# Kernel tuning notes

Measured on AMD Instinct MI355X. Metric: run time of the kernel, lower is better.

## Reference

```python
import jax, jax.numpy as jnp
import numpy as np

N_SRC_F = 40000; N_TGT_F = 40000; N_F = N_SRC_F + N_TGT_F
N_SRC_C = 1024; N_TGT_C = 1024; N_C = N_SRC_C + N_TGT_C
NN = 30        # KPConv neighbors per point
K = 15         # kernel points
C1 = 128       # fine-level feats (first_feats_dim)
C2 = 256       # coarse encoder out dim
GNN = 256      # gnn_feats_dim
HEADS = 4
DGCNN_K = 10
FINAL = 32     # final_feats_dim
EXT_F = 1.0; EXT_C = 2.0   # KPConv influence extents (scaled to unit-cube clouds)
EPS = 1e-12


def kpconv(q_pts, s_pts, s_feats, neighb, kpts, W, extent):
    # q_pts [Nq,3], s_pts [Ns,3], s_feats [Ns,Cin], neighb [Nq,NN], kpts [K,3], W [K,Cin,Cout]
    npts = s_pts[neighb]                              # [Nq,NN,3] irregular gather
    rel = npts - q_pts[:, None, :]
    # ||rel - kp||^2 expanded to avoid a [Nq,NN,K,3] intermediate
    d2 = (jnp.sum(rel * rel, -1)[:, :, None] + jnp.sum(kpts * kpts, -1)[None, None, :]
          - 2.0 * jnp.einsum('njd,kd->njk', rel, kpts))
    infl = jax.nn.relu(1.0 - jnp.sqrt(jnp.maximum(d2, EPS)) / extent)   # [Nq,NN,K]
    nf = s_feats[neighb]                              # [Nq,NN,Cin]
    h = jnp.einsum('njk,njc->nkc', infl, nf)          # kernel-point aggregation
    return jnp.einsum('nkc,kcd->nd', h, W)


def knn_idx(coords, k):
    sq = jnp.sum(coords * coords, -1)
    d2 = sq[:, None] + sq[None, :] - 2.0 * (coords @ coords.T)
    return jax.lax.top_k(-d2, k)[1]


def self_layer(coords, x, W, b):
    # DGCNN edge conv: knn on coords, edge = [x_i, x_j - x_i], 1x1 conv + relu, max over k
    idx = knn_idx(coords, DGCNN_K)
    neigh = x[idx]                                    # [N,k,C]
    ctr = jnp.broadcast_to(x[:, None, :], neigh.shape)
    edge = jnp.concatenate([ctr, neigh - ctr], -1)    # [N,k,2C]
    return jnp.max(jax.nn.relu(edge @ W + b), axis=1)


def cross_layer(x, y, Wq, Wk, Wv, Wm, bm):
    # multi-head cross attention x <- y, residual MLP on [x, message]
    N, C = x.shape
    dh = C // HEADS
    q = (x @ Wq).reshape(N, HEADS, dh)
    k = (y @ Wk).reshape(-1, HEADS, dh)
    v = (y @ Wv).reshape(-1, HEADS, dh)
    attn = jax.nn.softmax(jnp.einsum('nhd,mhd->hnm', q, k) / float(np.sqrt(dh)), axis=-1)
    msg = jnp.einsum('hnm,mhd->nhd', attn, v).reshape(N, C)
    return x + jnp.concatenate([x, msg], -1) @ Wm + bm


def l2norm(x):
    return x / jnp.maximum(jnp.linalg.norm(x, axis=1, keepdims=True), EPS)


def _forward(points_f, points_c, features, kernel_points_f, kernel_points_c,
             W_kp1, W_kp2, W_bottle, b_bottle, W_self1, b_self1,
             Wq, Wk, Wv, W_cross, b_cross, W_self2, b_self2,
             W_proj, b_proj, W_score, b_score, epsilon, W_dec, b_dec,
             neighbors_f, pool_idx, upsample_idx, len_src_c):
    # --- encoder: fine KPConv + strided KPConv to coarse ---
    x_f = kpconv(points_f, points_f, features, neighbors_f, kernel_points_f, W_kp1, EXT_F)  # [N_f,C1]
    skip = x_f
    x_c = kpconv(points_c, points_f, x_f, pool_idx, kernel_points_c, W_kp2, EXT_C)          # [N_c,C2]
    feats_c = x_c @ W_bottle + b_bottle                # bottleneck 1x1 conv -> [N_c,GNN]
    src, tgt = feats_c[:len_src_c], feats_c[len_src_c:]
    sc, tc = points_c[:len_src_c], points_c[len_src_c:]
    # --- GCN: self -> cross -> self (weights shared across src/tgt) ---
    src = self_layer(sc, src, W_self1, b_self1)
    tgt = self_layer(tc, tgt, W_self1, b_self1)
    src2 = cross_layer(src, tgt, Wq, Wk, Wv, W_cross, b_cross)
    tgt2 = cross_layer(tgt, src, Wq, Wk, Wv, W_cross, b_cross)
    src = self_layer(sc, src2, W_self2, b_self2)
    tgt = self_layer(tc, tgt2, W_self2, b_self2)
    feats = jnp.concatenate([src, tgt], 0) @ W_proj + b_proj   # proj_gnn
    scores_c_raw = feats @ W_score + b_score                   # proj_score [N_c,1]
    feats_norm = l2norm(feats)
    # --- bidirectional temperature-softmax matching head ---
    ip = feats_norm[:len_src_c] @ feats_norm[len_src_c:].T     # [Ns,Nt]
    temperature = jnp.exp(epsilon) + 0.03
    s1 = jax.nn.softmax(ip / temperature, axis=1) @ scores_c_raw[len_src_c:]
    s2 = jax.nn.softmax(ip.T / temperature, axis=1) @ scores_c_raw[:len_src_c]
    scores_saliency = jnp.concatenate([s1, s2], 0)
    # condition=True, add_cross_overlap=True branch
    x = jnp.concatenate([scores_c_raw, scores_saliency, feats], 1)    # [N_c, GNN+2]
    # --- decoder: nearest upsample + skip concat + unary conv ---
    x = jnp.concatenate([x[upsample_idx], skip], 1)            # [N_f, GNN+2+C1]
    x = x @ W_dec + b_dec                                      # [N_f, FINAL+2]
    feats_f = l2norm(x[:, :FINAL])
    so = jnp.clip(jax.nn.sigmoid(x[:, FINAL]), 0.0, 1.0)
    ss = jnp.clip(jax.nn.sigmoid(x[:, FINAL + 1]), 0.0, 1.0)
    so = jnp.where(jnp.isnan(so) | jnp.isinf(so), 0.0, so)     # regular_score
    ss = jnp.where(jnp.isnan(ss) | jnp.isinf(ss), 0.0, ss)
    return feats_f, so, ss


def _p(k, shape, fan):
    return jax.random.normal(k, shape, jnp.float32) / float(np.sqrt(fan))


def setup_inputs() -> dict:
    key = jax.random.key(0)
    ks = jax.random.split(key, 24)
    inp = {}
    inp['points_f'] = jax.random.uniform(ks[0], (N_F, 3), jnp.float32)
    inp['points_c'] = jax.random.uniform(ks[1], (N_C, 3), jnp.float32)
    inp['features'] = jnp.ones((N_F, 1), jnp.float32)
    inp['kernel_points_f'] = jax.random.normal(ks[2], (K, 3), jnp.float32) * 0.3
    inp['kernel_points_c'] = jax.random.normal(ks[3], (K, 3), jnp.float32) * 0.6
    inp['W_kp1'] = _p(ks[4], (K, 1, C1), K)
    inp['W_kp2'] = _p(ks[5], (K, C1, C2), K * C1)
    inp['W_bottle'] = _p(ks[6], (C2, GNN), C2); inp['b_bottle'] = jnp.zeros((GNN,), jnp.float32)
    inp['W_self1'] = _p(ks[7], (2 * GNN, GNN), 2 * GNN); inp['b_self1'] = jnp.zeros((GNN,), jnp.float32)
    inp['Wq'] = _p(ks[8], (GNN, GNN), GNN)
    inp['Wk'] = _p(ks[9], (GNN, GNN), GNN)
    inp['Wv'] = _p(ks[10], (GNN, GNN), GNN)
    inp['W_cross'] = _p(ks[11], (2 * GNN, GNN), 2 * GNN); inp['b_cross'] = jnp.zeros((GNN,), jnp.float32)
    inp['W_self2'] = _p(ks[12], (2 * GNN, GNN), 2 * GNN); inp['b_self2'] = jnp.zeros((GNN,), jnp.float32)
    inp['W_proj'] = _p(ks[13], (GNN, GNN), GNN); inp['b_proj'] = jnp.zeros((GNN,), jnp.float32)
    inp['W_score'] = _p(ks[14], (GNN, 1), GNN); inp['b_score'] = jnp.zeros((1,), jnp.float32)
    inp['epsilon'] = jnp.array(-5.0, jnp.float32)
    inp['W_dec'] = _p(ks[15], (GNN + 2 + C1, FINAL + 2), GNN + 2 + C1); inp['b_dec'] = jnp.zeros((FINAL + 2,), jnp.float32)
    inp['neighbors_f'] = jax.random.randint(ks[16], (N_F, NN), 0, N_F)
    inp['pool_idx'] = jax.random.randint(ks[17], (N_C, NN), 0, N_F)
    inp['upsample_idx'] = jax.random.randint(ks[18], (N_F,), 0, N_C)
    inp['len_src_c'] = N_SRC_C
    inp['len_src_f'] = N_SRC_F
    return inp


def reference(points_f, points_c, features, kernel_points_f, kernel_points_c,
              W_kp1, W_kp2, W_bottle, b_bottle, W_self1, b_self1,
              Wq, Wk, Wv, W_cross, b_cross, W_self2, b_self2,
              W_proj, b_proj, W_score, b_score, epsilon, W_dec, b_dec,
              neighbors_f, pool_idx, upsample_idx, len_src_c, len_src_f):
    return _forward(points_f, points_c, features, kernel_points_f, kernel_points_c,
                    W_kp1, W_kp2, W_bottle, b_bottle, W_self1, b_self1,
                    Wq, Wk, Wv, W_cross, b_cross, W_self2, b_self2,
                    W_proj, b_proj, W_score, b_score, epsilon, W_dec, b_dec,
                    neighbors_f, pool_idx, upsample_idx, len_src_c)
```

## Files before the change

kernel.cpp:

```cpp
#include <hip/hip_runtime.h>
#include <math.h>

#define NFINE   80000
#define NCRS    2048
#define NSRC    1024
#define NNB     30
#define KP      15
#define C1D     128
#define C2D     256
#define GD      256
#define DGK     10
#define FINALD  32
#define DECOUT  34

#define NCHUNK  8
#define CHUNK   128
#define TK      16
#define KC      4
#define KSTEP   480
#define GTR     16

__global__ __launch_bounds__(256) void kpconv_fine(
    const float* __restrict__ pts, const float* __restrict__ feat,
    const int* __restrict__ nbr, const float* __restrict__ kp,
    const float* __restrict__ W, float* __restrict__ out)
{
    int t = threadIdx.x, w = t >> 6, lane = t & 63;
    int n = blockIdx.x * 4 + w;
    __shared__ float contrib[4][NNB][17];
    __shared__ float h[4][KP + 1];
    float kx[KP], ky[KP], kz[KP], kk[KP];
#pragma unroll
    for (int k = 0; k < KP; k++) {
        kx[k] = kp[k*3]; ky[k] = kp[k*3+1]; kz[k] = kp[k*3+2];
        kk[k] = kx[k]*kx[k] + ky[k]*ky[k] + kz[k]*kz[k];
    }
    if (lane < NNB) {
        float qx = pts[n*3], qy = pts[n*3+1], qz = pts[n*3+2];
        int id = nbr[n*NNB + lane];
        float rx = pts[id*3]-qx, ry = pts[id*3+1]-qy, rz = pts[id*3+2]-qz;
        float rr = rx*rx + ry*ry + rz*rz;
        float f = feat[id];
#pragma unroll
        for (int k = 0; k < KP; k++) {
            float d2 = rr + kk[k] - 2.f*(rx*kx[k] + ry*ky[k] + rz*kz[k]);
            float infl = fmaxf(1.f - sqrtf(fmaxf(d2, 1e-12f)), 0.f);
            contrib[w][lane][k] = infl * f;
        }
    }
    __syncthreads();
    if (lane < KP) {
        float s = 0.f;
#pragma unroll
        for (int j = 0; j < NNB; j++) s += contrib[w][j][lane];
        h[w][lane] = s;
    }
    __syncthreads();
    float a0 = 0.f, a1 = 0.f;
#pragma unroll
    for (int k = 0; k < KP; k++) {
        float hk = h[w][k];
        a0 += hk * W[k*C1D + lane];
        a1 += hk * W[k*C1D + 64 + lane];
    }
    out[(size_t)n*C1D + lane]      = a0;
    out[(size_t)n*C1D + 64 + lane] = a1;
}

__global__ __launch_bounds__(256) void hh_kernel(
    const float* __restrict__ pc, const float* __restrict__ pf,
    const float* __restrict__ xf, const int* __restrict__ pool,
    const float* __restrict__ kp, float* __restrict__ hhg)
{
    int n = blockIdx.x, t = threadIdx.x;
    __shared__ float kx[KP], ky[KP], kz[KP], kk[KP];
    __shared__ float rel[NNB][4];
    __shared__ int   ids[NNB];
    __shared__ float infl[NNB][KP + 1];
    __shared__ float nf[NNB][C1D];
    if (t < KP) {
        float a = kp[t*3], b = kp[t*3+1], c = kp[t*3+2];
        kx[t] = a; ky[t] = b; kz[t] = c; kk[t] = a*a + b*b + c*c;
    }
    if (t < NNB) {
        int id = pool[n*NNB + t]; ids[t] = id;
        float qx = pc[n*3], qy = pc[n*3+1], qz = pc[n*3+2];
        float rx = pf[id*3]-qx, ry = pf[id*3+1]-qy, rz = pf[id*3+2]-qz;
        rel[t][0] = rx; rel[t][1] = ry; rel[t][2] = rz;
        rel[t][3] = rx*rx + ry*ry + rz*rz;
    }
    __syncthreads();
    for (int i = t; i < NNB*KP; i += 256) {
        int j = i / KP, kq = i % KP;
        float d2 = rel[j][3] + kk[kq]
                 - 2.f*(rel[j][0]*kx[kq] + rel[j][1]*ky[kq] + rel[j][2]*kz[kq]);
        infl[j][kq] = fmaxf(1.f - sqrtf(fmaxf(d2, 1e-12f)) * 0.5f, 0.f);
    }
    for (int i = t; i < NNB*C1D; i += 256) {
        int j = i >> 7, c = i & 127;
        nf[j][c] = xf[(size_t)ids[j]*C1D + c];
    }
    __syncthreads();
    for (int i = t; i < KP*C1D; i += 256) {
        int kq = i >> 7, c = i & 127;
        float s = 0.f;
#pragma unroll
        for (int j = 0; j < NNB; j++) s += infl[j][kq] * nf[j][c];
        hhg[(size_t)n*(KP*C1D) + i] = s;
    }
}

__global__ __launch_bounds__(256) void hh_gemm(
    const float* __restrict__ hhg, const float* __restrict__ W,
    float* __restrict__ pbuf)
{
    int t = threadIdx.x;
    int rg = blockIdx.x >> 2, kc = blockIdx.x & 3;
    int n0 = rg * GTR, kb0 = kc * KSTEP;
    __shared__ float xi[GTR][KSTEP];
    float* xf = &xi[0][0];
    for (int i = t; i < GTR*KSTEP; i += 256) {
        int r = i / KSTEP, c = i - r*KSTEP;
        xf[i] = hhg[(size_t)(n0 + r)*(KP*C1D) + kb0 + c];
    }
    __syncthreads();
    float a[GTR];
#pragma unroll
    for (int r = 0; r < GTR; r++) a[r] = 0.f;
    for (int c = 0; c < KSTEP; c += 4) {
        float w0 = W[(size_t)(kb0+c+0)*C2D + t];
        float w1 = W[(size_t)(kb0+c+1)*C2D + t];
        float w2 = W[(size_t)(kb0+c+2)*C2D + t];
        float w3 = W[(size_t)(kb0+c+3)*C2D + t];
#pragma unroll
        for (int r = 0; r < GTR; r++) {
            float4 xv = *(const float4*)&xi[r][c];
            a[r] += xv.x*w0 + xv.y*w1 + xv.z*w2 + xv.w*w3;
        }
    }
#pragma unroll
    for (int r = 0; r < GTR; r++)
        pbuf[(size_t)kc*NCRS*C2D + (size_t)(n0+r)*C2D + t] = a[r];
}

__global__ __launch_bounds__(256) void bottle_fused(
    const float* __restrict__ pbuf, const float* __restrict__ Wb,
    const float* __restrict__ b, float* __restrict__ out)
{
    int t = threadIdx.x, n0 = blockIdx.x * 4;
    const size_t MN = (size_t)NCRS*C2D;
    __shared__ float xi[4][C2D];
    for (int i = t; i < 4*C2D; i += 256) {
        int r = i >> 8, c = i & 255;
        size_t off = (size_t)(n0+r)*C2D + c;
        xi[r][c] = pbuf[off] + pbuf[MN+off] + pbuf[2*MN+off] + pbuf[3*MN+off];
    }
    __syncthreads();
    float a[4];
#pragma unroll
    for (int r = 0; r < 4; r++) a[r] = 0.f;
    for (int c = 0; c < C2D; c += 4) {
        float w0 = Wb[(c+0)*GD + t];
        float w1 = Wb[(c+1)*GD + t];
        float w2 = Wb[(c+2)*GD + t];
        float w3 = Wb[(c+3)*GD + t];
#pragma unroll
        for (int r = 0; r < 4; r++) {
            float4 xv = *(const float4*)&xi[r][c];
            a[r] += xv.x*w0 + xv.y*w1 + xv.z*w2 + xv.w*w3;
        }
    }
    float bv = b[t];
#pragma unroll
    for (int r = 0; r < 4; r++) out[(size_t)(n0+r)*GD + t] = a[r] + bv;
}

__global__ __launch_bounds__(512) void self_gemm(
    const float* __restrict__ x, const float* __restrict__ W,
    float* __restrict__ Y)
{
    int t = threadIdx.x, n0 = blockIdx.x * 4;
    __shared__ float xi[4][GD];
    for (int i = t; i < 4*GD; i += 512) {
        int r = i >> 8, c = i & 255;
        xi[r][c] = x[(size_t)(n0+r)*GD + c];
    }
    __syncthreads();
    const float* wcol = (t < GD) ? (W + t) : (W + (size_t)GD*GD + (t - GD));
    float a[4];
#pragma unroll
    for (int r = 0; r < 4; r++) a[r] = 0.f;
    for (int c = 0; c < GD; c += 4) {
        float w0 = wcol[(size_t)(c+0)*GD];
        float w1 = wcol[(size_t)(c+1)*GD];
        float w2 = wcol[(size_t)(c+2)*GD];
        float w3 = wcol[(size_t)(c+3)*GD];
#pragma unroll
        for (int r = 0; r < 4; r++) {
            float4 xv = *(const float4*)&xi[r][c];
            a[r] += xv.x*w0 + xv.y*w1 + xv.z*w2 + xv.w*w3;
        }
    }
#pragma unroll
    for (int r = 0; r < 4; r++) Y[(size_t)(n0+r)*512 + t] = a[r];
}

__global__ __launch_bounds__(256) void edge_max(
    const float* __restrict__ Y, const int* __restrict__ knn,
    const float* __restrict__ b, float* __restrict__ out)
{
    int n = blockIdx.x, t = threadIdx.x;
    int base = (n < NSRC) ? 0 : NSRC;
    __shared__ int ids[DGK];
    if (t < DGK) ids[t] = base + knn[n*DGK + t];
    __syncthreads();
    float a  = Y[(size_t)n*512 + t];
    float bn = Y[(size_t)n*512 + GD + t];
    float cst = a - bn + b[t];
    float acc = 0.f;
#pragma unroll
    for (int j = 0; j < DGK; j++) {
        float bj = Y[(size_t)ids[j]*512 + GD + t];
        acc = fmaxf(acc, fmaxf(cst + bj, 0.f));
    }
    out[(size_t)n*GD + t] = acc;
}

__global__ __launch_bounds__(256) void qkv_kernel(
    const float* __restrict__ x, const float* __restrict__ Wq,
    const float* __restrict__ Wk, const float* __restrict__ Wv,
    float* __restrict__ qb, float* __restrict__ kb, float* __restrict__ vb)
{
    int t = threadIdx.x, n0 = blockIdx.x * 4;
    __shared__ float xi[4][GD];
    for (int i = t; i < 4*GD; i += 256) {
        int r = i >> 8, c = i & 255;
        xi[r][c] = x[(size_t)(n0+r)*GD + c];
    }
    __syncthreads();
    const float* Ws[3] = {Wq, Wk, Wv};
    float* outs[3] = {qb, kb, vb};
#pragma unroll
    for (int m = 0; m < 3; m++) {
        const float* W = Ws[m];
        float a[4];
#pragma unroll
        for (int r = 0; r < 4; r++) a[r] = 0.f;
        for (int c = 0; c < GD; c += 4) {
            float w0 = W[(c+0)*GD + t];
            float w1 = W[(c+1)*GD + t];
            float w2 = W[(c+2)*GD + t];
            float w3 = W[(c+3)*GD + t];
#pragma unroll
            for (int r = 0; r < 4; r++) {
                float4 xv = *(const float4*)&xi[r][c];
                a[r] += xv.x*w0 + xv.y*w1 + xv.z*w2 + xv.w*w3;
            }
        }
        float* o = outs[m];
#pragma unroll
        for (int r = 0; r < 4; r++) o[(size_t)(n0+r)*GD + t] = a[r];
    }
}

__global__ __launch_bounds__(256) void knn_kernel(
    const float* __restrict__ pts, int* __restrict__ knn)
{
    int g = blockIdx.x;
    int t = threadIdx.x;
    int base = (g < NSRC) ? 0 : NSRC;
    int local = g - base;
    const float* P = pts + (size_t)base*3;
    __shared__ float d2s[NSRC];
    __shared__ float wval[4];
    __shared__ int   widx[4];
    float qx = P[local*3], qy = P[local*3+1], qz = P[local*3+2];
    float sqn = qx*qx + qy*qy + qz*qz;
#pragma unroll
    for (int ii = 0; ii < 4; ii++) {
        int m = t + ii*256;
        float px = P[m*3], py = P[m*3+1], pz = P[m*3+2];
        float sqm = px*px + py*py + pz*pz;
        d2s[m] = sqn + sqm - 2.f*(qx*px + qy*py + qz*pz);
    }
    __syncthreads();
    for (int r = 0; r < DGK; r++) {
        float bv = 3.4e38f; int bidx = NSRC;
#pragma unroll
        for (int ii = 0; ii < 4; ii++) {
            int m = t + ii*256;
            float v = d2s[m];
            if (v < bv) { bv = v; bidx = m; }
        }
#pragma unroll
        for (int off = 32; off >= 1; off >>= 1) {
            float ov = __shfl_xor(bv, off);
            int   oi = __shfl_xor(bidx, off);
            if (ov < bv || (ov == bv && oi < bidx)) { bv = ov; bidx = oi; }
        }
        if ((t & 63) == 0) { wval[t >> 6] = bv; widx[t >> 6] = bidx; }
        __syncthreads();
        if (t == 0) {
            float fv = wval[0]; int fi = widx[0];
#pragma unroll
            for (int wv2 = 1; wv2 < 4; wv2++)
                if (wval[wv2] < fv || (wval[wv2] == fv && widx[wv2] < fi)) {
                    fv = wval[wv2]; fi = widx[wv2];
                }
            knn[g*DGK + r] = fi;
            d2s[fi] = 3.4e38f;
        }
        __syncthreads();
    }
}

__global__ __launch_bounds__(256) void attn_flash(
    const float* __restrict__ qb, const float* __restrict__ kb,
    const float* __restrict__ vb, float* __restrict__ pm,
    float* __restrict__ pl, float* __restrict__ pacc)
{
    int bidx = blockIdx.x;
    int h = bidx & 3, chunk = (bidx >> 2) & 7, rb = bidx >> 5;
    int t = threadIdx.x;
    int u = t >> 2, li = t & 3;
    int row0 = rb * 128 + u * 2;
    int kbase = (row0 < NSRC) ? NSRC : 0;

    __shared__ float4 kt[2][TK][16];
    __shared__ float4 vt[2][TK][16];

    const float4* kb4 = (const float4*)kb;
    const float4* vb4 = (const float4*)vb;
    size_t gbase = ((size_t)(kbase + chunk*CHUNK)) * 64 + h*16;

    float4 q0[4], q1[4];
    const float4* qa = (const float4*)(qb + (size_t)row0*GD + h*64 + li*16);
    const float4* qc = (const float4*)(qb + (size_t)(row0+1)*GD + h*64 + li*16);
#pragma unroll
    for (int i = 0; i < 4; i++) { q0[i] = qa[i]; q1[i] = qc[i]; }
    float4 a0[4], a1[4];
#pragma unroll
    for (int i = 0; i < 4; i++) {
        a0[i] = make_float4(0.f, 0.f, 0.f, 0.f);
        a1[i] = make_float4(0.f, 0.f, 0.f, 0.f);
    }
    float mr0 = -INFINITY, lr0 = 0.f, mr1 = -INFINITY, lr1 = 0.f;
    float p0[TK], p1[TK];

    int f = t;
    float4 rk, rv;
    {
        size_t tb = gbase;
        rk = kb4[tb + (size_t)(f>>4)*64 + (f&15)];
        rv = vb4[tb + (size_t)(f>>4)*64 + (f&15)];
        kt[0][f>>4][f&15] = rk;
        vt[0][f>>4][f&15] = rv;
    }
    __syncthreads();

    const int NT = CHUNK / TK;
    for (int tile = 0; tile < NT; tile++) {
        int cur = tile & 1;
        if (tile + 1 < NT) {
            size_t tb = gbase + (size_t)(tile+1)*TK*64;
            rk = kb4[tb + (size_t)(f>>4)*64 + (f&15)];
            rv = vb4[tb + (size_t)(f>>4)*64 + (f&15)];
        }
        float tm0 = -INFINITY, tm1 = -INFINITY;
#pragma unroll
        for (int j = 0; j < TK; j++) {
            float4 k0 = kt[cur][j][li*4+0];
            float4 k1 = kt[cur][j][li*4+1];
            float4 k2 = kt[cur][j][li*4+2];
            float4 k3 = kt[cur][j][li*4+3];
            float pA = q0[0].x*k0.x + q0[0].y*k0.y + q0[0].z*k0.z + q0[0].w*k0.w
                     + q0[1].x*k1.x + q0[1].y*k1.y + q0[1].z*k1.z + q0[1].w*k1.w
                     + q0[2].x*k2.x + q0[2].y*k2.y + q0[2].z*k2.z + q0[2].w*k2.w
                     + q0[3].x*k3.x + q0[3].y*k3.y + q0[3].z*k3.z + q0[3].w*k3.w;
            float pB = q1[0].x*k0.x + q1[0].y*k0.y + q1[0].z*k0.z + q1[0].w*k0.w
                     + q1[1].x*k1.x + q1[1].y*k1.y + q1[1].z*k1.z + q1[1].w*k1.w
                     + q1[2].x*k2.x + q1[2].y*k2.y + q1[2].z*k2.z + q1[2].w*k2.w
                     + q1[3].x*k3.x + q1[3].y*k3.y + q1[3].z*k3.z + q1[3].w*k3.w;
            pA += __shfl_xor(pA, 1);  pB += __shfl_xor(pB, 1);
            pA += __shfl_xor(pA, 2);  pB += __shfl_xor(pB, 2);
            pA *= 0.125f;  pB *= 0.125f;
            p0[j] = pA;  p1[j] = pB;
            tm0 = fmaxf(tm0, pA);  tm1 = fmaxf(tm1, pB);
        }
        float mn0 = fmaxf(mr0, tm0), mn1 = fmaxf(mr1, tm1);
        float sc0 = __expf(mr0 - mn0), sc1 = __expf(mr1 - mn1);
        lr0 *= sc0;  lr1 *= sc1;
#pragma unroll
        for (int i = 0; i < 4; i++) {
            a0[i].x *= sc0; a0[i].y *= sc0; a0[i].z *= sc0; a0[i].w *= sc0;
            a1[i].x *= sc1; a1[i].y *= sc1; a1[i].z *= sc1; a1[i].w *= sc1;
        }
        mr0 = mn0;  mr1 = mn1;
#pragma unroll
        for (int j = 0; j < TK; j++) {
            float e0 = __expf(p0[j] - mn0);
            float e1 = __expf(p1[j] - mn1);
            lr0 += e0;  lr1 += e1;
            float4 v0 = vt[cur][j][li*4+0];
            float4 v1 = vt[cur][j][li*4+1];
            float4 v2 = vt[cur][j][li*4+2];
            float4 v3 = vt[cur][j][li*4+3];
            a0[0].x += e0*v0.x; a0[0].y += e0*v0.y; a0[0].z += e0*v0.z; a0[0].w += e0*v0.w;
            a0[1].x += e0*v1.x; a0[1].y += e0*v1.y; a0[1].z += e0*v1.z; a0[1].w += e0*v1.w;
            a0[2].x += e0*v2.x; a0[2].y += e0*v2.y; a0[2].z += e0*v2.z; a0[2].w += e0*v2.w;
            a0[3].x += e0*v3.x; a0[3].y += e0*v3.y; a0[3].z += e0*v3.z; a0[3].w += e0*v3.w;
            a1[0].x += e1*v0.x; a1[0].y += e1*v0.y; a1[0].z += e1*v0.z; a1[0].w += e1*v0.w;
            a1[1].x += e1*v1.x; a1[1].y += e1*v1.y; a1[1].z += e1*v1.z; a1[1].w += e1*v1.w;
            a1[2].x += e1*v2.x; a1[2].y += e1*v2.y; a1[2].z += e1*v2.z; a1[2].w += e1*v2.w;
            a1[3].x += e1*v3.x; a1[3].y += e1*v3.y; a1[3].z += e1*v3.z; a1[3].w += e1*v3.w;
        }
        if (tile + 1 < NT) {
            __syncthreads();
            int nb = (tile + 1) & 1;
            kt[nb][f>>4][f&15] = rk;
            vt[nb][f>>4][f&15] = rv;
            __syncthreads();
        }
    }
    int pi0 = (chunk*4 + h)*NCRS + row0;
    if (li == 0) { pm[pi0] = mr0; pl[pi0] = lr0; pm[pi0+1] = mr1; pl[pi0+1] = lr1; }
    float4* po0 = (float4*)(pacc + (size_t)pi0*64);
    float4* po1 = (float4*)(pacc + (size_t)(pi0+1)*64);
#pragma unroll
    for (int i = 0; i < 4; i++) { po0[li*4 + i] = a0[i]; po1[li*4 + i] = a1[i]; }
}

__global__ __launch_bounds__(256) void cross_fused(
    const float* __restrict__ x, const float* __restrict__ pm,
    const float* __restrict__ pl, const float* __restrict__ pacc,
    const float* __restrict__ Wm, const float* __restrict__ bm,
    float* __restrict__ out)
{
    int t = threadIdx.x, n0 = blockIdx.x * 4;
    int h = t >> 6, d = t & 63;
    __shared__ float xs[4][GD], ms[4][GD];
    for (int i = t; i < 4*GD; i += 256) {
        int r = i >> 8, c = i & 255;
        xs[r][c] = x[(size_t)(n0+r)*GD + c];
    }
#pragma unroll
    for (int r = 0; r < 4; r++) {
        int row = n0 + r;
        float m = -INFINITY;
#pragma unroll
        for (int c = 0; c < NCHUNK; c++) m = fmaxf(m, pm[(c*4 + h)*NCRS + row]);
        float lsum = 0.f, asum = 0.f;
#pragma unroll
        for (int c = 0; c < NCHUNK; c++) {
            int pi = (c*4 + h)*NCRS + row;
            float w = __expf(pm[pi] - m);
            lsum += pl[pi] * w;
            asum += pacc[(size_t)pi*64 + d] * w;
        }
        ms[r][t] = asum / lsum;
    }
    __syncthreads();
    float bv = bm[t];
    float a[4] = {bv, bv, bv, bv};
    for (int c = 0; c < GD; c += 4) {
        float w10 = Wm[(c+0)*GD + t];
        float w11 = Wm[(c+1)*GD + t];
        float w12 = Wm[(c+2)*GD + t];
        float w13 = Wm[(c+3)*GD + t];
        float w20 = Wm[(GD+c+0)*GD + t];
        float w21 = Wm[(GD+c+1)*GD + t];
        float w22 = Wm[(GD+c+2)*GD + t];
        float w23 = Wm[(GD+c+3)*GD + t];
#pragma unroll
        for (int r = 0; r < 4; r++) {
            float4 xv = *(const float4*)&xs[r][c];
            float4 mv = *(const float4*)&ms[r][c];
            a[r] += xv.x*w10 + xv.y*w11 + xv.z*w12 + xv.w*w13
                  + mv.x*w20 + mv.y*w21 + mv.z*w22 + mv.w*w23;
        }
    }
#pragma unroll
    for (int r = 0; r < 4; r++)
        out[(size_t)(n0+r)*GD + t] = xs[r][t] + a[r];
}

__global__ __launch_bounds__(256) void proj_norm(
    const float* __restrict__ x, const float* __restrict__ W,
    const float* __restrict__ b, const float* __restrict__ Wsc,
    const float* __restrict__ bsc, float* __restrict__ feats,
    float* __restrict__ fnorm, float* __restrict__ scores)
{
    int t = threadIdx.x, n0 = blockIdx.x * 4;
    __shared__ float xi[4][GD];
    __shared__ float pf[4][GD];
    for (int i = t; i < 4*GD; i += 256) {
        int r = i >> 8, c = i & 255;
        xi[r][c] = x[(size_t)(n0+r)*GD + c];
    }
    __syncthreads();
    float a[4] = {0.f, 0.f, 0.f, 0.f};
    for (int c = 0; c < GD; c += 4) {
        float w0 = W[(c+0)*GD + t];
        float w1 = W[(c+1)*GD + t];
        float w2 = W[(c+2)*GD + t];
        float w3 = W[(c+3)*GD + t];
#pragma unroll
        for (int r = 0; r < 4; r++) {
            float4 xv = *(const float4*)&xi[r][c];
            a[r] += xv.x*w0 + xv.y*w1 + xv.z*w2 + xv.w*w3;
        }
    }
    float bv = b[t];
#pragma unroll
    for (int r = 0; r < 4; r++) {
        float v = a[r] + bv;
        feats[(size_t)(n0+r)*GD + t] = v;
        pf[r][t] = v;
    }
    __syncthreads();
    int lane = t & 63, w = t >> 6;
    int rr = n0 + w;
    float q0 = pf[w][lane], q1 = pf[w][64+lane], q2 = pf[w][128+lane], q3 = pf[w][192+lane];
    float sq = q0*q0 + q1*q1 + q2*q2 + q3*q3;
    float sc = q0*Wsc[lane] + q1*Wsc[64+lane] + q2*Wsc[128+lane] + q3*Wsc[192+lane];
#pragma unroll
    for (int off = 32; off >= 1; off >>= 1) {
        sq += __shfl_xor(sq, off);
        sc += __shfl_xor(sc, off);
    }
    float inv = 1.f / fmaxf(sqrtf(sq), 1e-12f);
    fnorm[(size_t)rr*GD + lane]       = q0*inv;
    fnorm[(size_t)rr*GD + 64 + lane]  = q1*inv;
    fnorm[(size_t)rr*GD + 128 + lane] = q2*inv;
    fnorm[(size_t)rr*GD + 192 + lane] = q3*inv;
    if (lane == 0) scores[rr] = sc + bsc[0];
}

__global__ __launch_bounds__(256) void ip_kernel(
    const float* __restrict__ fnorm, float* __restrict__ ip)
{
    int t = threadIdx.x;
    int n0 = (blockIdx.x >> 2) * 4;
    int m  = (blockIdx.x & 3) * 256 + t;
    __shared__ float xs[GD][4];
    for (int i = t; i < 4*GD; i += 256) {
        int r = i >> 8, c = i & 255;
        xs[c][r] = fnorm[(size_t)(n0+r)*GD + c];
    }
    __syncthreads();
    const float4* fr = (const float4*)(fnorm + (size_t)(NSRC + m)*GD);
    float a0 = 0.f, a1 = 0.f, a2 = 0.f, a3 = 0.f;
    for (int c4 = 0; c4 < GD/4; c4++) {
        float4 f = fr[c4];
        float4 xa = *(const float4*)&xs[c4*4+0][0];
        float4 xb = *(const float4*)&xs[c4*4+1][0];
        float4 xc = *(const float4*)&xs[c4*4+2][0];
        float4 xd = *(const float4*)&xs[c4*4+3][0];
        a0 += f.x*xa.x + f.y*xb.x + f.z*xc.x + f.w*xd.x;
        a1 += f.x*xa.y + f.y*xb.y + f.z*xc.y + f.w*xd.y;
        a2 += f.x*xa.z + f.y*xb.z + f.z*xc.z + f.w*xd.z;
        a3 += f.x*xa.w + f.y*xb.w + f.z*xc.w + f.w*xd.w;
    }
    ip[(size_t)(n0+0)*NSRC + m] = a0;
    ip[(size_t)(n0+1)*NSRC + m] = a1;
    ip[(size_t)(n0+2)*NSRC + m] = a2;
    ip[(size_t)(n0+3)*NSRC + m] = a3;
}

__global__ __launch_bounds__(256) void saliency_all(
    const float* __restrict__ ip, const float* __restrict__ scores,
    const float* __restrict__ epsv, float* __restrict__ sal_out)
{
    int g = blockIdx.x, t = threadIdx.x;
    bool col = (g >= NSRC);
    int n = col ? (g - NSRC) : g;
    const float* so = col ? scores : (scores + NSRC);
    float T = expf(epsv[0]) + 0.03f;
    __shared__ float red[256];
    float vals[4];
    float m = -INFINITY;
#pragma unroll
    for (int ii = 0; ii < 4; ii++) {
        int i = t + ii*256;
        float vv = col ? ip[(size_t)i*NSRC + n] : ip[(size_t)n*NSRC + i];
        vv /= T;
        vals[ii] = vv;
        m = fmaxf(m, vv);
    }
    red[t] = m; __syncthreads();
    for (int s = 128; s > 0; s >>= 1) { if (t < s) red[t] = fmaxf(red[t], red[t+s]); __syncthreads(); }
    float mx = red[0]; __syncthreads();
    float se = 0.f, wsum = 0.f;
#pragma unroll
    for (int ii = 0; ii < 4; ii++) {
        int i = t + ii*256;
        float e = expf(vals[ii] - mx);
        se += e; wsum += e * so[i];
    }
    red[t] = se; __syncthreads();
    for (int s = 128; s > 0; s >>= 1) { if (t < s) red[t] += red[t+s]; __syncthreads(); }
    float S = red[0]; __syncthreads();
    red[t] = wsum; __syncthreads();
    for (int s = 128; s > 0; s >>= 1) { if (t < s) red[t] += red[t+s]; __syncthreads(); }
    if (t == 0) sal_out[g] = red[0] / S;
}

__global__ __launch_bounds__(256) void dec_coarse(
    const float* __restrict__ scores, const float* __restrict__ sal,
    const float* __restrict__ feats, const float* __restrict__ Wd,
    const float* __restrict__ bd, float* __restrict__ decfeat)
{
    int t = threadIdx.x, lane = t & 63, w = t >> 6;
    int n = blockIdx.x * 4 + w;
    __shared__ float xr[4][GD];
    for (int c = lane; c < GD; c += 64) xr[w][c] = feats[(size_t)n*GD + c];
    float acc = 0.f;
    if (lane < DECOUT) {
        acc = bd[lane] + scores[n]*Wd[lane] + sal[n]*Wd[DECOUT + lane];
        for (int c = 0; c < GD; c++) acc += xr[w][c] * Wd[(2 + c)*DECOUT + lane];
    }
    if (lane < 40) decfeat[(size_t)n*40 + lane] = (lane < DECOUT) ? acc : 0.f;
}

__global__ __launch_bounds__(256) void decoder_kernel(
    const float* __restrict__ decfeat, const float* __restrict__ skip,
    const int* __restrict__ ups, const float* __restrict__ Wd,
    float* __restrict__ outf, float* __restrict__ outso,
    float* __restrict__ outss)
{
    int t = threadIdx.x;
    __shared__ float wsk[C1D*36];
    for (int i = t; i < C1D*36; i += 256) {
        int cc = i / 36, j = i - cc*36;
        wsk[i] = (j < DECOUT) ? Wd[(size_t)(2 + GD + cc)*DECOUT + j] : 0.f;
    }
    __syncthreads();
    int row = blockIdx.x * 256 + t;
    if (row >= NFINE) return;
    int u = ups[row];
    float4 acc[9];
    const float4* df = (const float4*)(decfeat + (size_t)u*40);
#pragma unroll
    for (int q = 0; q < 9; q++) acc[q] = df[q];
    const float4* sr = (const float4*)(skip + (size_t)row*C1D);
    for (int c4 = 0; c4 < C1D/4; c4++) {
        float4 xv = sr[c4];
        const float* wb = wsk + c4*4*36;
#pragma unroll
        for (int q = 0; q < 9; q++) {
            float4 w0 = *(const float4*)&wb[q*4];
            float4 w1 = *(const float4*)&wb[36 + q*4];
            float4 w2 = *(const float4*)&wb[72 + q*4];
            float4 w3 = *(const float4*)&wb[108 + q*4];
            acc[q].x += xv.x*w0.x + xv.y*w1.x + xv.z*w2.x + xv.w*w3.x;
            acc[q].y += xv.x*w0.y + xv.y*w1.y + xv.z*w2.y + xv.w*w3.y;
            acc[q].z += xv.x*w0.z + xv.y*w1.z + xv.z*w2.z + xv.w*w3.z;
            acc[q].w += xv.x*w0.w + xv.y*w1.w + xv.z*w2.w + xv.w*w3.w;
        }
    }
    float sq = 0.f;
#pragma unroll
    for (int q = 0; q < 8; q++)
        sq += acc[q].x*acc[q].x + acc[q].y*acc[q].y + acc[q].z*acc[q].z + acc[q].w*acc[q].w;
    float inv = 1.f / fmaxf(sqrtf(sq), 1e-12f);
    float4* op = (float4*)(outf + (size_t)row*FINALD);
#pragma unroll
    for (int q = 0; q < 8; q++)
        op[q] = make_float4(acc[q].x*inv, acc[q].y*inv, acc[q].z*inv, acc[q].w*inv);
    float so = 1.f/(1.f + __expf(-acc[8].x));
    so = fminf(fmaxf(so, 0.f), 1.f); if (!(so == so)) so = 0.f;
    float ss = 1.f/(1.f + __expf(-acc[8].y));
    ss = fminf(fmaxf(ss, 0.f), 1.f); if (!(ss == ss)) ss = 0.f;
    outso[row] = so; outss[row] = ss;
}

extern "C" void kernel_launch(void* const* d_in, const int* in_sizes, int n_in,
                              void* d_out, int out_size, void* d_ws, size_t ws_size,
                              hipStream_t stream)
{
    const float* points_f     = (const float*)d_in[0];
    const float* points_c     = (const float*)d_in[1];
    const float* features     = (const float*)d_in[2];
    const float* kp_f         = (const float*)d_in[3];
    const float* kp_c         = (const float*)d_in[4];
    const float* W_kp1        = (const float*)d_in[5];
    const float* W_kp2        = (const float*)d_in[6];
    const float* W_bottle     = (const float*)d_in[7];
    const float* b_bottle     = (const float*)d_in[8];
    const float* W_self1      = (const float*)d_in[9];
    const float* b_self1      = (const float*)d_in[10];
    const float* Wq           = (const float*)d_in[11];
    const float* Wk           = (const float*)d_in[12];
    const float* Wv           = (const float*)d_in[13];
    const float* W_cross      = (const float*)d_in[14];
    const float* b_cross      = (const float*)d_in[15];
    const float* W_self2      = (const float*)d_in[16];
    const float* b_self2      = (const float*)d_in[17];
    const float* W_proj       = (const float*)d_in[18];
    const float* b_proj       = (const float*)d_in[19];
    const float* W_score      = (const float*)d_in[20];
    const float* b_score      = (const float*)d_in[21];
    const float* epsilon      = (const float*)d_in[22];
    const float* W_dec        = (const float*)d_in[23];
    const float* b_dec        = (const float*)d_in[24];
    const int*   neighbors_f  = (const int*)d_in[25];
    const int*   pool_idx     = (const int*)d_in[26];
    const int*   upsample_idx = (const int*)d_in[27];

    float* ws = (float*)d_ws;
    size_t o = 0;
    auto alloc = [&](size_t nfl) { float* p = ws + o; o += (nfl + 63) & ~(size_t)63; return p; };
    float* x_f     = alloc((size_t)NFINE * C1D);
    float* g1      = alloc((size_t)NCRS * GD);
    float* qb      = alloc((size_t)NCRS * GD);
    float* kb      = alloc((size_t)NCRS * GD);
    float* vb      = alloc((size_t)NCRS * GD);
    float* feats_c = alloc((size_t)NCRS * GD);
    float* scores  = alloc(NCRS);
    float* sal     = alloc(NCRS);
    float* decfeat = alloc((size_t)NCRS * 40);
    int*   knn_b   = (int*)alloc(NCRS * DGK);

    const size_t NG = (size_t)NCRS * GD;
    const size_t MN = (size_t)NCRS * C2D;
    const size_t PMN = (size_t)NCRS * 4 * NCHUNK;
    size_t usz = 4*MN + (size_t)NCRS*KP*C1D;
    float* U = alloc(usz);
    float* pbuf = U;
    float* hhg  = U + 4*MN;
    float* Y1   = U;
    float* pm   = U;
    float* pl   = U + PMN;
    float* pacc = U + 2*PMN;
    float* g2   = U + 2*PMN + PMN*64;
    float* Y2   = U;
    float* g3   = U + 2*NG;
    float* feats= U + 3*NG;
    float* fnorm= U + 4*NG;
    float* ip   = U + 5*NG;
    
    float* outf  = (float*)d_out;
    float* outso = outf + (size_t)NFINE * FINALD;
    float* outss = outso + NFINE;

    kpconv_fine<<<NFINE/4, 256, 0, stream>>>(points_f, features, neighbors_f, kp_f, W_kp1, x_f);
    hh_kernel<<<NCRS, 256, 0, stream>>>(points_c, points_f, x_f, pool_idx, kp_c, hhg);
    hh_gemm<<<(NCRS/GTR)*KC, 256, 0, stream>>>(hhg, W_kp2, pbuf);
    bottle_fused<<<NCRS/4, 256, 0, stream>>>(pbuf, W_bottle, b_bottle, feats_c);

    knn_kernel<<<NCRS, 256, 0, stream>>>(points_c, knn_b);
    self_gemm<<<NCRS/4, 512, 0, stream>>>(feats_c, W_self1, Y1);
    edge_max<<<NCRS, 256, 0, stream>>>(Y1, knn_b, b_self1, g1);
    qkv_kernel<<<NCRS/4, 256, 0, stream>>>(g1, Wq, Wk, Wv, qb, kb, vb);
    attn_flash<<<512, 256, 0, stream>>>(qb, kb, vb, pm, pl, pacc);
    cross_fused<<<NCRS/4, 256, 0, stream>>>(g1, pm, pl, pacc, W_cross, b_cross, g2);
    self_gemm<<<NCRS/4, 512, 0, stream>>>(g2, W_self2, Y2);
    edge_max<<<NCRS, 256, 0, stream>>>(Y2, knn_b, b_self2, g3);

    proj_norm<<<NCRS/4, 256, 0, stream>>>(g3, W_proj, b_proj, W_score, b_score,
                                          feats, fnorm, scores);
    ip_kernel<<<NSRC, 256, 0, stream>>>(fnorm, ip);
    saliency_all<<<NCRS, 256, 0, stream>>>(ip, scores, epsilon, sal);

    dec_coarse<<<NCRS/4, 256, 0, stream>>>(scores, sal, feats, W_dec, b_dec, decfeat);
    decoder_kernel<<<(NFINE + 255)/256, 256, 0, stream>>>(decfeat, x_f, upsample_idx,
                                                          W_dec, outf, outso, outss);
}
```

Before: 470.7 us.

## Rework flash-attention thread mapping to 4 rows per thread group and smaller key tiles

Changes the attention kernel so each group of 8 lanes handles 4 query rows with 8 dims each, instead of 4 lanes handling 2 rows with 16 dims. Shared-memory K/V loads are reused across more rows, and the key tile shrinks so half the threads stage K and half stage V. The aim is fewer LDS reads per FLOP and lower register pressure. In exchange it adds an extra shuffle stage per dot product and twice as many tile iterations with barriers.

```diff
diff --git a/kernel.cpp b/kernel.cpp
--- a/kernel.cpp
+++ b/kernel.cpp
@@ -15,7 +15,7 @@
 
 #define NCHUNK  8
 #define CHUNK   128
-#define TK      16
+#define TK      8
 #define KC      4
 #define KSTEP   480
 #define GTR     16
@@ -322,8 +322,8 @@
     int bidx = blockIdx.x;
     int h = bidx & 3, chunk = (bidx >> 2) & 7, rb = bidx >> 5;
     int t = threadIdx.x;
-    int u = t >> 2, li = t & 3;
-    int row0 = rb * 128 + u * 2;
+    int u = t >> 3, li = t & 7;
+    int row0 = rb * 128 + u * 4;
     int kbase = (row0 < NSRC) ? NSRC : 0;
 
     __shared__ float4 kt[2][TK][16];
@@ -333,101 +333,90 @@
     const float4* vb4 = (const float4*)vb;
     size_t gbase = ((size_t)(kbase + chunk*CHUNK)) * 64 + h*16;
 
-    float4 q0[4], q1[4];
-    const float4* qa = (const float4*)(qb + (size_t)row0*GD + h*64 + li*16);
-    const float4* qc = (const float4*)(qb + (size_t)(row0+1)*GD + h*64 + li*16);
-#pragma unroll
-    for (int i = 0; i < 4; i++) { q0[i] = qa[i]; q1[i] = qc[i]; }
-    float4 a0[4], a1[4];
-#pragma unroll
-    for (int i = 0; i < 4; i++) {
-        a0[i] = make_float4(0.f, 0.f, 0.f, 0.f);
-        a1[i] = make_float4(0.f, 0.f, 0.f, 0.f);
-    }
-    float mr0 = -INFINITY, lr0 = 0.f, mr1 = -INFINITY, lr1 = 0.f;
-    float p0[TK], p1[TK];
-
-    int f = t;
-    float4 rk, rv;
-    {
-        size_t tb = gbase;
-        rk = kb4[tb + (size_t)(f>>4)*64 + (f&15)];
-        rv = vb4[tb + (size_t)(f>>4)*64 + (f&15)];
-        kt[0][f>>4][f&15] = rk;
-        vt[0][f>>4][f&15] = rv;
-    }
+    float4 q[4][2];
+#pragma unroll
+    for (int r = 0; r < 4; r++) {
+        const float4* qp = (const float4*)(qb + (size_t)(row0+r)*GD + h*64 + li*8);
+        q[r][0] = qp[0]; q[r][1] = qp[1];
+    }
+    float4 a[4][2];
+#pragma unroll
+    for (int r = 0; r < 4; r++) {
+        a[r][0] = make_float4(0.f,0.f,0.f,0.f);
+        a[r][1] = make_float4(0.f,0.f,0.f,0.f);
+    }
+    float mr[4], lr[4], p[4][TK];
+#pragma unroll
+    for (int r = 0; r < 4; r++) { mr[r] = -INFINITY; lr[r] = 0.f; }
+
+    int half = t >> 7, sidx = t & 127, skey = sidx >> 4, scomp = sidx & 15;
+    const float4* sb = half ? vb4 : kb4;
+    float4 rs = sb[gbase + (size_t)skey*64 + scomp];
+    if (half) vt[0][skey][scomp] = rs; else kt[0][skey][scomp] = rs;
     __syncthreads();
 
     const int NT = CHUNK / TK;
     for (int tile = 0; tile < NT; tile++) {
         int cur = tile & 1;
-        if (tile + 1 < NT) {
-            size_t tb = gbase + (size_t)(tile+1)*TK*64;
-            rk = kb4[tb + (size_t)(f>>4)*64 + (f&15)];
-            rv = vb4[tb + (size_t)(f>>4)*64 + (f&15)];
-        }
-        float tm0 = -INFINITY, tm1 = -INFINITY;
+        if (tile + 1 < NT)
+            rs = sb[gbase + (size_t)(tile+1)*TK*64 + (size_t)skey*64 + scomp];
+        float tm[4];
+#pragma unroll
+        for (int r = 0; r < 4; r++) tm[r] = -INFINITY;
 #pragma unroll
         for (int j = 0; j < TK; j++) {
-            float4 k0 = kt[cur][j][li*4+0];
-            float4 k1 = kt[cur][j][li*4+1];
-            float4 k2 = kt[cur][j][li*4+2];
-            float4 k3 = kt[cur][j][li*4+3];
-            float pA = q0[0].x*k0.x + q0[0].y*k0.y + q0[0].z*k0.z + q0[0].w*k0.w
-                     + q0[1].x*k1.x + q0[1].y*k1.y + q0[1].z*k1.z + q0[1].w*k1.w
-                     + q0[2].x*k2.x + q0[2].y*k2.y + q0[2].z*k2.z + q0[2].w*k2.w
-                     + q0[3].x*k3.x + q0[3].y*k3.y + q0[3].z*k3.z + q0[3].w*k3.w;
-            float pB = q1[0].x*k0.x + q1[0].y*k0.y + q1[0].z*k0.z + q1[0].w*k0.w
-                     + q1[1].x*k1.x + q1[1].y*k1.y + q1[1].z*k1.z + q1[1].w*k1.w
-                     + q1[2].x*k2.x + q1[2].y*k2.y + q1[2].z*k2.z + q1[2].w*k2.w
-                     + q1[3].x*k3.x + q1[3].y*k3.y + q1[3].z*k3.z + q1[3].w*k3.w;
-            pA += __shfl_xor(pA, 1);  pB += __shfl_xor(pB, 1);
-            pA += __shfl_xor(pA, 2);  pB += __shfl_xor(pB, 2);
-            pA *= 0.125f;  pB *= 0.125f;
-            p0[j] = pA;  p1[j] = pB;
-            tm0 = fmaxf(tm0, pA);  tm1 = fmaxf(tm1, pB);
-        }
-        float mn0 = fmaxf(mr0, tm0), mn1 = fmaxf(mr1, tm1);
-        float sc0 = __expf(mr0 - mn0), sc1 = __expf(mr1 - mn1);
-        lr0 *= sc0;  lr1 *= sc1;
-#pragma unroll
-        for (int i = 0; i < 4; i++) {
-            a0[i].x *= sc0; a0[i].y *= sc0; a0[i].z *= sc0; a0[i].w *= sc0;
-            a1[i].x *= sc1; a1[i].y *= sc1; a1[i].z *= sc1; a1[i].w *= sc1;
-        }
-        mr0 = mn0;  mr1 = mn1;
+            float4 k0 = kt[cur][j][li*2+0];
+            float4 k1 = kt[cur][j][li*2+1];
+#pragma unroll
+            for (int r = 0; r < 4; r++) {
+                float pp = q[r][0].x*k0.x + q[r][0].y*k0.y + q[r][0].z*k0.z + q[r][0].w*k0.w
+                         + q[r][1].x*k1.x + q[r][1].y*k1.y + q[r][1].z*k1.z + q[r][1].w*k1.w;
+                pp += __shfl_xor(pp, 1);
+                pp += __shfl_xor(pp, 2);
+                pp += __shfl_xor(pp, 4);
+                pp *= 0.125f;
+                p[r][j] = pp;
+                tm[r] = fmaxf(tm[r], pp);
+            }
+        }
+#pragma unroll
+        for (int r = 0; r < 4; r++) {
+            float mn = fmaxf(mr[r], tm[r]);
+            float sc = __expf(mr[r] - mn);
+            lr[r] *= sc;
+            a[r][0].x *= sc; a[r][0].y *= sc; a[r][0].z *= sc; a[r][0].w *= sc;
+            a[r][1].x *= sc; a[r][1].y *= sc; a[r][1].z *= sc; a[r][1].w *= sc;
+            mr[r] = mn;
+        }
 #pragma unroll
         for (int j = 0; j < TK; j++) {
-            float e0 = __expf(p0[j] - mn0);
-            float e1 = __expf(p1[j] - mn1);
-            lr0 += e0;  lr1 += e1;
-            float4 v0 = vt[cur][j][li*4+0];
-            float4 v1 = vt[cur][j][li*4+1];
-            float4 v2 = vt[cur][j][li*4+2];
-            float4 v3 = vt[cur][j][li*4+3];
-            a0[0].x += e0*v0.x; a0[0].y += e0*v0.y; a0[0].z += e0*v0.z; a0[0].w += e0*v0.w;
-            a0[1].x += e0*v1.x; a0[1].y += e0*v1.y; a0[1].z += e0*v1.z; a0[1].w += e0*v1.w;
-            a0[2].x += e0*v2.x; a0[2].y += e0*v2.y; a0[2].z += e0*v2.z; a0[2].w += e0*v2.w;
-            a0[3].x += e0*v3.x; a0[3].y += e0*v3.y; a0[3].z += e0*v3.z; a0[3].w += e0*v3.w;
-            a1[0].x += e1*v0.x; a1[0].y += e1*v0.y; a1[0].z += e1*v0.z; a1[0].w += e1*v0.w;
-            a1[1].x += e1*v1.x; a1[1].y += e1*v1.y; a1[1].z += e1*v1.z; a1[1].w += e1*v1.w;
-            a1[2].x += e1*v2.x; a1[2].y += e1*v2.y; a1[2].z += e1*v2.z; a1[2].w += e1*v2.w;
-            a1[3].x += e1*v3.x; a1[3].y += e1*v3.y; a1[3].z += e1*v3.z; a1[3].w += e1*v3.w;
+            float4 v0 = vt[cur][j][li*2+0];
+            float4 v1 = vt[cur][j][li*2+1];
+#pragma unroll
+            for (int r = 0; r < 4; r++) {
+                float e = __expf(p[r][j] - mr[r]);
+                lr[r] += e;
+                a[r][0].x += e*v0.x; a[r][0].y += e*v0.y;
+                a[r][0].z += e*v0.z; a[r][0].w += e*v0.w;
+                a[r][1].x += e*v1.x; a[r][1].y += e*v1.y;
+                a[r][1].z += e*v1.z; a[r][1].w += e*v1.w;
+            }
         }
         if (tile + 1 < NT) {
             __syncthreads();
-            int nb = (tile + 1) & 1;
-            kt[nb][f>>4][f&15] = rk;
-            vt[nb][f>>4][f&15] = rv;
+            if (half) vt[(tile+1)&1][skey][scomp] = rs;
+            else      kt[(tile+1)&1][skey][scomp] = rs;
             __syncthreads();
         }
     }
-    int pi0 = (chunk*4 + h)*NCRS + row0;
-    if (li == 0) { pm[pi0] = mr0; pl[pi0] = lr0; pm[pi0+1] = mr1; pl[pi0+1] = lr1; }
-    float4* po0 = (float4*)(pacc + (size_t)pi0*64);
-    float4* po1 = (float4*)(pacc + (size_t)(pi0+1)*64);
-#pragma unroll
-    for (int i = 0; i < 4; i++) { po0[li*4 + i] = a0[i]; po1[li*4 + i] = a1[i]; }
+#pragma unroll
+    for (int r = 0; r < 4; r++) {
+        int pi = (chunk*4 + h)*NCRS + row0 + r;
+        if (li == 0) { pm[pi] = mr[r]; pl[pi] = lr[r]; }
+        float4* po = (float4*)(pacc + (size_t)pi*64);
+        po[li*2+0] = a[r][0];
+        po[li*2+1] = a[r][1];
+    }
 }
 
 __global__ __launch_bounds__(256) void cross_fused(
@@ -738,7 +727,7 @@
     float* feats= U + 3*NG;
     float* fnorm= U + 4*NG;
     float* ip   = U + 5*NG;
-    
+
     float* outf  = (float*)d_out;
     float* outso = outf + (size_t)NFINE * FINALD;
     float* outss = outso + NFINE;
```

Result: no change. 462.3 us (-1.8%).
